# Performance work log

Measured on AMD Instinct MI355X. Metric: run time of the kernel, lower is better.

The kernel has to match this reference:

```python
import jax, jax.numpy as jnp
import numpy as np
import math

EPS = 1e-12


def _cmul(ar, ai, br, bi):
    return ar * br - ai * bi, ar * bi + ai * br


def _wilson_seed(x):
    # x: (B, 4, L, L) -> conj of canonical Wilson-line path, (B, L, L) re/im
    ux_r, ux_i, uy_r, uy_i = x[:, 0], x[:, 1], x[:, 2], x[:, 3]
    B, L, _ = ux_r.shape
    dt = x.dtype

    def step(c, u):
        cr, ci = c
        ur, ui = u
        nr, ni = _cmul(cr, ci, ur, ui)
        return (nr, ni), (nr, ni)

    # cumulative complex product along x at y=0
    init_r = jnp.ones((B,), dt)
    init_i = jnp.zeros((B,), dt)
    xs = (ux_r[:, :-1, 0].T, ux_i[:, :-1, 0].T)  # (L-1, B)
    _, (axr, axi) = jax.lax.scan(step, (init_r, init_i), xs)
    x_axis_r = jnp.concatenate([init_r[None], axr], 0).T  # (B, L)
    x_axis_i = jnp.concatenate([init_i[None], axi], 0).T

    # cumulative complex product along y, vectorized over x
    ys = (jnp.moveaxis(uy_r[:, :, :-1], 2, 0), jnp.moveaxis(uy_i[:, :, :-1], 2, 0))  # (L-1, B, L)
    _, (pr, pi_) = jax.lax.scan(step, (x_axis_r, x_axis_i), ys)
    path_r = jnp.moveaxis(jnp.concatenate([x_axis_r[None], pr], 0), 0, 2)  # (B, L, L)
    path_i = jnp.moveaxis(jnp.concatenate([x_axis_i[None], pi_], 0), 0, 2)
    return path_r, -path_i  # conjugate


def _wrap(t):
    return (t + math.pi) % (2.0 * math.pi) - math.pi


def _initial_features(x):
    seed_r, seed_i = _wilson_seed(x)
    ax = jnp.arctan2(x[:, 1], x[:, 0])
    ay = jnp.arctan2(x[:, 3], x[:, 2])
    plaq = _wrap(ax + jnp.roll(ay, -1, axis=1) - jnp.roll(ax, -1, axis=2) - ay)
    pc = jnp.cos(plaq)
    pavg = (pc + jnp.roll(pc, 1, 1) + jnp.roll(pc, -1, 1)
            + jnp.roll(pc, 1, 2) + jnp.roll(pc, -1, 2)) / 5.0
    scalars = jnp.stack([jnp.ones_like(pc), pc, pavg], axis=1)  # (B, 3, L, L)
    return seed_r[:, None] * scalars, seed_i[:, None] * scalars


def _transport_fwd(fr, fi, x, mu):
    lr, li = (x[:, 0], x[:, 1]) if mu == 0 else (x[:, 2], x[:, 3])
    sr = jnp.roll(fr, -1, axis=mu + 2)
    si = jnp.roll(fi, -1, axis=mu + 2)
    return _cmul(lr[:, None], li[:, None], sr, si)


def _transport_bwd(fr, fi, x, mu):
    lr, li = (x[:, 0], x[:, 1]) if mu == 0 else (x[:, 2], x[:, 3])
    cr = jnp.roll(lr, 1, axis=mu + 1)
    ci = jnp.roll(-li, 1, axis=mu + 1)
    sr = jnp.roll(fr, 1, axis=mu + 2)
    si = jnp.roll(fi, 1, axis=mu + 2)
    return _cmul(cr[:, None], ci[:, None], sr, si)


def _lconv(fr, fi, x, center, fwd_w, bwd_w):
    out_r = jnp.einsum('oi,bixy->boxy', center, fr)
    out_i = jnp.einsum('oi,bixy->boxy', center, fi)
    for mu in range(2):
        fr2, fi2 = _transport_fwd(fr, fi, x, mu)
        br2, bi2 = _transport_bwd(fr, fi, x, mu)
        out_r = out_r + jnp.einsum('oi,bixy->boxy', fwd_w[mu], fr2) \
                      + jnp.einsum('oi,bixy->boxy', bwd_w[mu], br2)
        out_i = out_i + jnp.einsum('oi,bixy->boxy', fwd_w[mu], fi2) \
                      + jnp.einsum('oi,bixy->boxy', bwd_w[mu], bi2)
    return out_r, out_i


def _modrelu(fr, fi, bias):
    mag = jnp.sqrt(fr * fr + fi * fi + EPS)
    act = jax.nn.relu(mag + bias[None, :, None, None])
    scale = act / jnp.maximum(mag, EPS)
    return fr * scale, fi * scale


def setup_inputs() -> dict:
    key = jax.random.key(0)
    ks = jax.random.split(key, 11)
    B, L, H, O = 64, 128, 16, 8
    s = 0.1
    return {
        'x': jax.random.normal(ks[0], (B, 4, L, L), jnp.float32),
        'center1': s * jax.random.normal(ks[1], (H, 3), jnp.float32),
        'fwd_w1': s * jax.random.normal(ks[2], (2, H, 3), jnp.float32),
        'bwd_w1': s * jax.random.normal(ks[3], (2, H, 3), jnp.float32),
        'bias1': jnp.zeros((H,), jnp.float32),
        'center2': s * jax.random.normal(ks[4], (O, H), jnp.float32),
        'fwd_w2': s * jax.random.normal(ks[5], (2, O, H), jnp.float32),
        'bwd_w2': s * jax.random.normal(ks[6], (2, O, H), jnp.float32),
        'bias2': jnp.zeros((O,), jnp.float32),
        'ro_weight': s * jax.random.normal(ks[7], (O,), jnp.float32),
        'ro_bias': jnp.zeros((1,), jnp.float32),
    }


def reference(x, center1, fwd_w1, bwd_w1, bias1, center2, fwd_w2, bwd_w2, bias2, ro_weight, ro_bias):
    fr, fi = _initial_features(x)
    fr, fi = _lconv(fr, fi, x, center1, fwd_w1, bwd_w1)
    fr, fi = _modrelu(fr, fi, bias1)
    fr, fi = _lconv(fr, fi, x, center2, fwd_w2, bwd_w2)
    fr, fi = _modrelu(fr, fi, bias2)
    inv = fr * fr + fi * fi
    return jnp.einsum('c,bcxy->bxy', ro_weight, inv)[:, None] + ro_bias.reshape(1, 1, 1, 1)
```

## Files before the change

kernel.cpp:

```cpp
#include <hip/hip_runtime.h>
#include <math.h>

#define LQ   128
#define BQ   64
#define LL   (LQ*LQ)
#define H1   16
#define O2   8
#define TILE 16
#define REG  18
#define NPTS (REG*REG)
#define PCR  22
#define PCN  (PCR*PCR)
#define LKR  23
#define LKN  (LKR*LKR)
#define SDR  20
#define SDN  (SDR*SDR)
#define FSTR 20

typedef float f2 __attribute__((ext_vector_type(2)));

__device__ __forceinline__ int wrapi(int v) { return v & (LQ - 1); }

__device__ __forceinline__ unsigned f2bf(float f) {
    unsigned u = __float_as_uint(f);
    u += 0x7fffu + ((u >> 16) & 1u);
    return u >> 16;
}

#define WS_W1 ((size_t)BQ * LL)

__global__ __launch_bounds__(256)
void k_scan(const float* __restrict__ x,
            const float* __restrict__ c1, const float* __restrict__ fw1,
            const float* __restrict__ bw1, float* __restrict__ ws) {
    int blk = blockIdx.x;
    if (blk == BQ * 8) {
        int tid = threadIdx.x;
        if (tid < 120) {
            int t = tid / 24, r = tid - t * 24;
            int c = r >> 3, op = r & 7;
            const float* src = (t == 0) ? c1 : (t == 1) ? fw1 : (t == 2) ? bw1
                             : (t == 3) ? (fw1 + 48) : (bw1 + 48);
            float2 v = make_float2(src[(2 * op) * 3 + c], src[(2 * op + 1) * 3 + c]);
            ((float2*)ws)[WS_W1 + tid] = v;
        }
        return;
    }
    int b = blk >> 3, rq = blk & 7;
    int l = threadIdx.x & 63, w = threadIdx.x >> 6;
    const float* x0 = x + (size_t)b * 4 * LL;
    const float* x1 = x0 + LL;

    float ur0 = x0[(2 * l) * LQ],     ui0 = x1[(2 * l) * LQ];
    float ur1 = x0[(2 * l + 1) * LQ], ui1 = x1[(2 * l + 1) * LQ];
    float pr = ur0 * ur1 - ui0 * ui1;
    float pi = ur0 * ui1 + ui0 * ur1;
    for (int d = 1; d < 64; d <<= 1) {
        float qr = __shfl_up(pr, d, 64);
        float qi = __shfl_up(pi, d, 64);
        if (l >= d) {
            float nr = qr * pr - qi * pi;
            float ni = qr * pi + qi * pr;
            pr = nr; pi = ni;
        }
    }
    float er = __shfl_up(pr, 1, 64);
    float ei = __shfl_up(pi, 1, 64);
    if (l == 0) { er = 1.f; ei = 0.f; }
    float e1r = er * ur0 - ei * ui0;
    float e1i = er * ui0 + ei * ur0;

    const float* yrp = x + (size_t)(b * 4 + 2) * LL;
    const float* yip = yrp + LL;
    float4* seed4 = (float4*)ws;

    for (int k = 0; k < 4; ++k) {
        int i = rq * 16 + w * 4 + k;
        float cxr = __shfl((i & 1) ? e1r : er, i >> 1, 64);
        float cxi = __shfl((i & 1) ? e1i : ei, i >> 1, 64);
        const float* yr = yrp + (size_t)i * LQ;
        const float* yi = yip + (size_t)i * LQ;
        float vr0 = yr[2 * l],     vi0 = yi[2 * l];
        float vr1 = yr[2 * l + 1], vi1 = yi[2 * l + 1];
        float sr = vr0 * vr1 - vi0 * vi1;
        float si = vr0 * vi1 + vi0 * vr1;
        for (int d = 1; d < 64; d <<= 1) {
            float qr = __shfl_up(sr, d, 64);
            float qi = __shfl_up(si, d, 64);
            if (l >= d) {
                float nr = qr * sr - qi * si;
                float ni = qr * si + qi * sr;
                sr = nr; si = ni;
            }
        }
        float gr = __shfl_up(sr, 1, 64);
        float gi = __shfl_up(si, 1, 64);
        if (l == 0) { gr = 1.f; gi = 0.f; }
        float s0r = cxr * gr - cxi * gi;
        float s0i = cxr * gi + cxi * gr;
        float s1r = s0r * vr0 - s0i * vi0;
        float s1i = s0r * vi0 + s0i * vr0;
        seed4[((size_t)b * LL + (size_t)i * LQ) / 2 + l] =
            make_float4(s0r, -s0i, s1r, -s1i);
    }
}

__global__ __launch_bounds__(256, 4)
void k_main(const float* __restrict__ x,
            const float* __restrict__ c2, const float* __restrict__ fw2,
            const float* __restrict__ bw2, const float* __restrict__ b1,
            const float* __restrict__ b2,
            const float* __restrict__ ro, const float* __restrict__ rob,
            const float* __restrict__ ws, float* __restrict__ out) {
    __shared__ unsigned s_f1[NPTS * FSTR];
    __shared__ f2 s_ux[LKN];
    __shared__ f2 s_uy[LKN];
    __shared__ float s_pc[PCN];
    __shared__ f2 s_sd[SDN];
    int tid = threadIdx.x;
    int b = blockIdx.z, i0 = blockIdx.y * TILE, j0 = blockIdx.x * TILE;
    const float* x0 = x + (size_t)b * 4 * LL;
    const float* x1 = x0 + LL;
    const float* x2 = x0 + 2 * LL;
    const float* x3 = x0 + 3 * LL;
    const float2* seed = (const float2*)ws + (size_t)b * LL;
    const float2* W1 = (const float2*)ws + WS_W1;

    for (int p = tid; p < LKN; p += 256) {
        int ri = p / LKR, rj = p - ri * LKR;
        int gi = wrapi(i0 - 3 + ri), gj = wrapi(j0 - 3 + rj);
        int idx = gi * LQ + gj;
        s_ux[p] = (f2){x0[idx], x1[idx]};
        s_uy[p] = (f2){x2[idx], x3[idx]};
    }
    for (int p = tid; p < SDN; p += 256) {
        int ri = p / SDR, rj = p - ri * SDR;
        int gi = wrapi(i0 - 2 + ri), gj = wrapi(j0 - 2 + rj);
        float2 s = seed[gi * LQ + gj];
        s_sd[p] = (f2){s.x, s.y};
    }
    __syncthreads();

    for (int p = tid; p < PCN; p += 256) {
        int ri = p / PCR, rj = p - ri * PCR;
        int lb = ri * LKR + rj;
        f2 u1 = s_ux[lb];
        f2 u2 = s_uy[lb + LKR];
        f2 u3 = s_ux[lb + 1];
        f2 u4 = s_uy[lb];
        float ar = u1.x * u2.x - u1.y * u2.y, ai = u1.x * u2.y + u1.y * u2.x;
        float br = ar * u3.x + ai * u3.y,     bi = -ar * u3.y + ai * u3.x;
        float zr = br * u4.x + bi * u4.y,     zi = -br * u4.y + bi * u4.x;
        s_pc[p] = zr * __frsqrt_rn(fmaf(zr, zr, zi * zi) + 1e-30f);
    }
    __syncthreads();

#pragma unroll
    for (int pass = 0; pass < 2; ++pass) {
        int p = tid + pass * 256;
        if (pass == 1 && p >= NPTS) break;
        int ri = p / REG, rj = p - ri * REG;
        int sc = (ri + 1) * SDR + (rj + 1);
        int lb = (ri + 2) * LKR + (rj + 2);
        int cb = (ri + 2) * PCR + (rj + 2);

        f2 t[5]; float tc[5], tv[5];
        {
            f2 SC = s_sd[sc], SXP = s_sd[sc + SDR], SXM = s_sd[sc - SDR];
            f2 SYP = s_sd[sc + 1], SYM = s_sd[sc - 1];
            f2 lx = s_ux[lb], ly = s_uy[lb];
            f2 mx = s_ux[lb - LKR], my = s_uy[lb - 1];
            t[0] = SC;
            t[1] = (f2){lx.x * SXP.x - lx.y * SXP.y, lx.x * SXP.y + lx.y * SXP.x};
            t[2] = (f2){mx.x * SXM.x + mx.y * SXM.y, mx.x * SXM.y - mx.y * SXM.x};
            t[3] = (f2){ly.x * SYP.x - ly.y * SYP.y, ly.x * SYP.y + ly.y * SYP.x};
            t[4] = (f2){my.x * SYM.x + my.y * SYM.y, my.x * SYM.y - my.y * SYM.x};
            int ct[5] = {cb, cb + PCR, cb - PCR, cb + 1, cb - 1};
#pragma unroll
            for (int q = 0; q < 5; ++q) {
                int c = ct[q];
                tc[q] = s_pc[c];
                tv[q] = (s_pc[c] + s_pc[c - PCR] + s_pc[c + PCR]
                       + s_pc[c - 1] + s_pc[c + 1]) * 0.2f;
            }
        }

        f2 accr[8], acci[8];
#pragma unroll
        for (int op = 0; op < 8; ++op) { accr[op] = (f2){0.f, 0.f}; acci[op] = (f2){0.f, 0.f}; }
#pragma unroll
        for (int q = 0; q < 5; ++q) {
            f2 tcv = (f2){tc[q], tc[q]}, tvv = (f2){tv[q], tv[q]};
            f2 trv = (f2){t[q].x, t[q].x}, tiv = (f2){t[q].y, t[q].y};
            const float2* Wq = W1 + q * 24;
#pragma unroll
            for (int op = 0; op < 8; ++op) {
                float2 w0 = Wq[op], w1 = Wq[8 + op], w2 = Wq[16 + op];
                f2 mp = (f2){w0.x, w0.y};
                mp += (f2){w1.x, w1.y} * tcv;
                mp += (f2){w2.x, w2.y} * tvv;
                accr[op] += mp * trv;
                acci[op] += mp * tiv;
            }
        }
        unsigned* fp = &s_f1[p * FSTR];
#pragma unroll
        for (int op = 0; op < 8; ++op) {
            f2 q2 = accr[op] * accr[op] + acci[op] * acci[op] + (f2){1e-12f, 1e-12f};
            float s0 = fmaxf(fmaf(b1[2 * op],     __frsqrt_rn(q2.x), 1.f), 0.f);
            float s1 = fmaxf(fmaf(b1[2 * op + 1], __frsqrt_rn(q2.y), 1.f), 0.f);
            f2 sv = (f2){s0, s1};
            f2 fr = accr[op] * sv, fi = acci[op] * sv;
            unsigned u0 = f2bf(fr.x) | (f2bf(fi.x) << 16);
            unsigned u1 = f2bf(fr.y) | (f2bf(fi.y) << 16);
            *(uint2*)&fp[2 * op] = make_uint2(u0, u1);
        }
    }
    __syncthreads();

    int ty = tid >> 4, tx = tid & 15;
    int i = i0 + ty, j = j0 + tx;
    int pos = (ty + 1) * REG + (tx + 1);
    int lb2 = (ty + 3) * LKR + (tx + 3);
    f2 lx = s_ux[lb2], ly = s_uy[lb2];
    f2 mx = s_ux[lb2 - LKR], my = s_uy[lb2 - 1];

    f2 a2[O2];
#pragma unroll
    for (int o = 0; o < O2; ++o) a2[o] = (f2){0.f, 0.f};

    const float* wt[5] = {c2, fw2, bw2, fw2 + O2 * H1, bw2 + O2 * H1};
    int   dp[5] = {0, REG, -REG, 1, -1};
    float lr[5] = {1.f, lx.x, mx.x,  ly.x, my.x};
    float li[5] = {0.f, lx.y, -mx.y, ly.y, -my.y};

#pragma unroll
    for (int q = 0; q < 5; ++q) {
        const unsigned* fp = &s_f1[(pos + dp[q]) * FSTR];
        unsigned dw[16];
#pragma unroll
        for (int k = 0; k < 4; ++k)
            *(uint4*)&dw[4 * k] = *(const uint4*)&fp[4 * k];
        const float* w = wt[q];
        f2 s[O2];
#pragma unroll
        for (int o = 0; o < O2; ++o) s[o] = (f2){0.f, 0.f};
#pragma unroll
        for (int h = 0; h < H1; ++h) {
            f2 f = (f2){__uint_as_float(dw[h] << 16),
                        __uint_as_float(dw[h] & 0xffff0000u)};
#pragma unroll
            for (int o = 0; o < O2; ++o) s[o] += w[o * H1 + h] * f;
        }
        f2 rot = (f2){-li[q], li[q]};
#pragma unroll
        for (int o = 0; o < O2; ++o) {
            f2 sw = (f2){s[o].y, s[o].x};
            a2[o] += lr[q] * s[o] + rot * sw;
        }
    }

    float res = rob[0];
#pragma unroll
    for (int o = 0; o < O2; ++o) {
        float q = fmaf(a2[o].x, a2[o].x, a2[o].y * a2[o].y);
        float s = fmaxf(fmaf(b2[o], __frsqrt_rn(q + 1e-12f), 1.f), 0.f);
        res = fmaf(ro[o], s * s * q, res);
    }
    out[(size_t)b * LL + i * LQ + j] = res;
}

extern "C" void kernel_launch(void* const* d_in, const int* in_sizes, int n_in,
                              void* d_out, int out_size, void* d_ws, size_t ws_size,
                              hipStream_t stream) {
    const float* x   = (const float*)d_in[0];
    const float* c1  = (const float*)d_in[1];
    const float* fw1 = (const float*)d_in[2];
    const float* bw1 = (const float*)d_in[3];
    const float* b1  = (const float*)d_in[4];
    const float* c2  = (const float*)d_in[5];
    const float* fw2 = (const float*)d_in[6];
    const float* bw2 = (const float*)d_in[7];
    const float* b2  = (const float*)d_in[8];
    const float* ro  = (const float*)d_in[9];
    const float* rob = (const float*)d_in[10];
    float* out = (float*)d_out;
    float* ws  = (float*)d_ws;

    k_scan<<<BQ * 8 + 1, 256, 0, stream>>>(x, c1, fw1, bw1, ws);
    dim3 grid(LQ / TILE, LQ / TILE, BQ);
    k_main<<<grid, 256, 0, stream>>>(x, c2, fw2, bw2, b1, b2,
                                     ro, rob, ws, out);
}
```

Before: 150.6 us.

## Use bf16 MFMA for second lconv and skip modReLU when biases are zero

Replaces the per-thread scalar second-layer channel mixing with 16x16x32 bf16 MFMA instructions, splitting layer-1 features into separate real/imag shared arrays so they load as MFMA B operands. Each wave processes four output rows and reduces results across quads with shuffles. It also adds runtime checks for all-zero biases and skips the modReLU normalisation when they are zero. The MFMA path wastes half the K dimension with zero padding and adds weight conversion per block.

```diff
diff --git a/kernel.cpp b/kernel.cpp
--- a/kernel.cpp
+++ b/kernel.cpp
@@ -15,9 +15,11 @@
 #define LKN  (LKR*LKR)
 #define SDR  20
 #define SDN  (SDR*SDR)
-#define FSTR 20
+#define FSTR 10
 
 typedef float f2 __attribute__((ext_vector_type(2)));
+using bf8 = __attribute__((ext_vector_type(8))) short;
+using f4  = __attribute__((ext_vector_type(4))) float;
 
 __device__ __forceinline__ int wrapi(int v) { return v & (LQ - 1); }
 
@@ -112,7 +114,8 @@
             const float* __restrict__ b2,
             const float* __restrict__ ro, const float* __restrict__ rob,
             const float* __restrict__ ws, float* __restrict__ out) {
-    __shared__ unsigned s_f1[NPTS * FSTR];
+    __shared__ unsigned s_f1r[NPTS * FSTR];
+    __shared__ unsigned s_f1i[NPTS * FSTR];
     __shared__ f2 s_ux[LKN];
     __shared__ f2 s_uy[LKN];
     __shared__ float s_pc[PCN];
@@ -126,6 +129,13 @@
     const float2* seed = (const float2*)ws + (size_t)b * LL;
     const float2* W1 = (const float2*)ws + WS_W1;
 
+    bool z1 = true;
+#pragma unroll
+    for (int h = 0; h < H1; ++h) z1 = z1 && (b1[h] == 0.f);
+    bool z2 = true;
+#pragma unroll
+    for (int o = 0; o < O2; ++o) z2 = z2 && (b2[o] == 0.f);
+
     for (int p = tid; p < LKN; p += 256) {
         int ri = p / LKR, rj = p - ri * LKR;
         int gi = wrapi(i0 - 3 + ri), gj = wrapi(j0 - 3 + rj);
@@ -203,71 +213,121 @@
                 acci[op] += mp * tiv;
             }
         }
-        unsigned* fp = &s_f1[p * FSTR];
-#pragma unroll
-        for (int op = 0; op < 8; ++op) {
-            f2 q2 = accr[op] * accr[op] + acci[op] * acci[op] + (f2){1e-12f, 1e-12f};
-            float s0 = fmaxf(fmaf(b1[2 * op],     __frsqrt_rn(q2.x), 1.f), 0.f);
-            float s1 = fmaxf(fmaf(b1[2 * op + 1], __frsqrt_rn(q2.y), 1.f), 0.f);
-            f2 sv = (f2){s0, s1};
-            f2 fr = accr[op] * sv, fi = acci[op] * sv;
-            unsigned u0 = f2bf(fr.x) | (f2bf(fi.x) << 16);
-            unsigned u1 = f2bf(fr.y) | (f2bf(fi.y) << 16);
-            *(uint2*)&fp[2 * op] = make_uint2(u0, u1);
+        if (!z1) {
+#pragma unroll
+            for (int op = 0; op < 8; ++op) {
+                f2 q2 = accr[op] * accr[op] + acci[op] * acci[op] + (f2){1e-12f, 1e-12f};
+                float s0 = fmaxf(fmaf(b1[2 * op],     __frsqrt_rn(q2.x), 1.f), 0.f);
+                float s1 = fmaxf(fmaf(b1[2 * op + 1], __frsqrt_rn(q2.y), 1.f), 0.f);
+                f2 sv = (f2){s0, s1};
+                accr[op] *= sv; acci[op] *= sv;
+            }
+        }
+        unsigned* fr_ = &s_f1r[p * FSTR];
+        unsigned* fi_ = &s_f1i[p * FSTR];
+#pragma unroll
+        for (int d = 0; d < 4; ++d) {
+            unsigned r0 = f2bf(accr[2*d].x)   | (f2bf(accr[2*d].y) << 16);
+            unsigned r1 = f2bf(accr[2*d+1].x) | (f2bf(accr[2*d+1].y) << 16);
+            unsigned i0_ = f2bf(acci[2*d].x)   | (f2bf(acci[2*d].y) << 16);
+            unsigned i1_ = f2bf(acci[2*d+1].x) | (f2bf(acci[2*d+1].y) << 16);
+            *(uint2*)&fr_[2*d] = make_uint2(r0, r1);
+            *(uint2*)&fi_[2*d] = make_uint2(i0_, i1_);
         }
     }
     __syncthreads();
 
-    int ty = tid >> 4, tx = tid & 15;
-    int i = i0 + ty, j = j0 + tx;
-    int pos = (ty + 1) * REG + (tx + 1);
-    int lb2 = (ty + 3) * LKR + (tx + 3);
-    f2 lx = s_ux[lb2], ly = s_uy[lb2];
-    f2 mx = s_ux[lb2 - LKR], my = s_uy[lb2 - 1];
-
-    f2 a2[O2];
-#pragma unroll
-    for (int o = 0; o < O2; ++o) a2[o] = (f2){0.f, 0.f};
-
-    const float* wt[5] = {c2, fw2, bw2, fw2 + O2 * H1, bw2 + O2 * H1};
-    int   dp[5] = {0, REG, -REG, 1, -1};
-    float lr[5] = {1.f, lx.x, mx.x,  ly.x, my.x};
-    float li[5] = {0.f, lx.y, -mx.y, ly.y, -my.y};
-
+    int lane = tid & 63, w = tid >> 6;
+    int quad = lane >> 4, nIdx = lane & 15;
+
+    const float* wt0 = c2;
+    const float* wt1 = fw2;
+    const float* wt2 = bw2;
+    const float* wt3 = fw2 + O2 * H1;
+    const float* wt4 = bw2 + O2 * H1;
+    const float* wts[5] = {wt0, wt1, wt2, wt3, wt4};
+    bf8 afr[5];
+    bool aval = (nIdx < O2) && (quad < 2);
 #pragma unroll
     for (int q = 0; q < 5; ++q) {
-        const unsigned* fp = &s_f1[(pos + dp[q]) * FSTR];
-        unsigned dw[16];
-#pragma unroll
-        for (int k = 0; k < 4; ++k)
-            *(uint4*)&dw[4 * k] = *(const uint4*)&fp[4 * k];
-        const float* w = wt[q];
-        f2 s[O2];
-#pragma unroll
-        for (int o = 0; o < O2; ++o) s[o] = (f2){0.f, 0.f};
-#pragma unroll
-        for (int h = 0; h < H1; ++h) {
-            f2 f = (f2){__uint_as_float(dw[h] << 16),
-                        __uint_as_float(dw[h] & 0xffff0000u)};
-#pragma unroll
-            for (int o = 0; o < O2; ++o) s[o] += w[o * H1 + h] * f;
-        }
-        f2 rot = (f2){-li[q], li[q]};
-#pragma unroll
-        for (int o = 0; o < O2; ++o) {
-            f2 sw = (f2){s[o].y, s[o].x};
-            a2[o] += lr[q] * s[o] + rot * sw;
-        }
-    }
-
-    float res = rob[0];
-#pragma unroll
-    for (int o = 0; o < O2; ++o) {
-        float q = fmaf(a2[o].x, a2[o].x, a2[o].y * a2[o].y);
-        float s = fmaxf(fmaf(b2[o], __frsqrt_rn(q + 1e-12f), 1.f), 0.f);
-        res = fmaf(ro[o], s * s * q, res);
-    }
-    out[(size_t)b * LL + i * LQ + j] = res;
+        bf8 z = {0, 0, 0, 0, 0, 0, 0, 0};
+        if (aval) {
+            const float* wp = wts[q] + nIdx * H1 + quad * 8;
+            float4 wa = *(const float4*)wp;
+            float4 wb = *(const float4*)(wp + 4);
+            uint4 u;
+            u.x = f2bf(wa.x) | (f2bf(wa.y) << 16);
+            u.y = f2bf(wa.z) | (f2bf(wa.w) << 16);
+            u.z = f2bf(wb.x) | (f2bf(wb.y) << 16);
+            u.w = f2bf(wb.z) | (f2bf(wb.w) << 16);
+            __builtin_memcpy(&z, &u, 16);
+        }
+        afr[q] = z;
+    }
+    float4 ro_lo = *(const float4*)ro;
+    float4 ro_hi = *(const float4*)(ro + 4);
+    float4 b2_lo = *(const float4*)b2;
+    float4 b2_hi = *(const float4*)(b2 + 4);
+    float4 zf4 = make_float4(0.f, 0.f, 0.f, 0.f);
+    float4 rv = (quad == 0) ? ro_lo : ((quad == 1) ? ro_hi : zf4);
+    float4 bv = (quad == 0) ? b2_lo : ((quad == 1) ? b2_hi : zf4);
+    float rob0 = rob[0];
+    const int dp5[5] = {0, REG, -REG, 1, -1};
+
+    for (int g = 0; g < 4; ++g) {
+        int row = w * 4 + g;
+        int posc = (row + 1) * REG + (nIdx + 1);
+        int lb2 = (row + 3) * LKR + (nIdx + 3);
+        f2 lx = s_ux[lb2], ly = s_uy[lb2];
+        f2 mx = s_ux[lb2 - LKR], my = s_uy[lb2 - 1];
+        float lrq[5] = {1.f, lx.x, mx.x,  ly.x, my.x};
+        float liq[5] = {0.f, lx.y, -mx.y, ly.y, -my.y};
+
+        f4 a2r = {0.f, 0.f, 0.f, 0.f}, a2i = {0.f, 0.f, 0.f, 0.f};
+#pragma unroll
+        for (int q = 0; q < 5; ++q) {
+            bf8 br = {0, 0, 0, 0, 0, 0, 0, 0};
+            bf8 bi = {0, 0, 0, 0, 0, 0, 0, 0};
+            if (quad < 2) {
+                int posq = posc + dp5[q];
+                const unsigned* pr_ = &s_f1r[posq * FSTR + quad * 4];
+                uint2 lo = *(const uint2*)pr_;
+                uint2 hi = *(const uint2*)(pr_ + 2);
+                uint4 ur = {lo.x, lo.y, hi.x, hi.y};
+                __builtin_memcpy(&br, &ur, 16);
+                const unsigned* pi_ = &s_f1i[posq * FSTR + quad * 4];
+                uint2 lo2 = *(const uint2*)pi_;
+                uint2 hi2 = *(const uint2*)(pi_ + 2);
+                uint4 ui = {lo2.x, lo2.y, hi2.x, hi2.y};
+                __builtin_memcpy(&bi, &ui, 16);
+            }
+            f4 zc = {0.f, 0.f, 0.f, 0.f};
+            f4 sr = __builtin_amdgcn_mfma_f32_16x16x32_bf16(afr[q], br, zc, 0, 0, 0);
+            f4 si = __builtin_amdgcn_mfma_f32_16x16x32_bf16(afr[q], bi, zc, 0, 0, 0);
+            a2r += lrq[q] * sr - liq[q] * si;
+            a2i += lrq[q] * si + liq[q] * sr;
+        }
+
+        f4 q4 = a2r * a2r + a2i * a2i;
+        float res;
+        if (z2) {
+            res = rv.x * q4.x + rv.y * q4.y + rv.z * q4.z + rv.w * q4.w;
+        } else {
+            float bvv[4] = {bv.x, bv.y, bv.z, bv.w};
+            float rvv[4] = {rv.x, rv.y, rv.z, rv.w};
+            res = 0.f;
+#pragma unroll
+            for (int r = 0; r < 4; ++r) {
+                float qq = q4[r];
+                float s = fmaxf(fmaf(bvv[r], __frsqrt_rn(qq + 1e-12f), 1.f), 0.f);
+                res = fmaf(rvv[r], s * s * qq, res);
+            }
+        }
+        res += __shfl_xor(res, 16, 64);
+        res += __shfl_xor(res, 32, 64);
+        if (quad == 0)
+            out[(size_t)b * LL + (size_t)(i0 + row) * LQ + (j0 + nIdx)] = res + rob0;
+    }
 }
 
 extern "C" void kernel_launch(void* const* d_in, const int* in_sizes, int n_in,
```

After: 145.4 us. -3.5%, faster.
